# Kernel tuning notes

Hardware: AMD Instinct MI355X
Metric: run time of the kernel (lower is better)

The kernel has to match this reference:

```python
import jax, jax.numpy as jnp
import numpy as np

B, P, K = 32, 1024, 20  # clouds, points per cloud, kNN neighbors
EPS = 1e-5


def knn_idx(x, k):
    # x: [B,P,d] -> indices of k nearest neighbors (squared L2, includes self), [B,P,k]
    d2 = jnp.sum(x * x, axis=-1)
    dist = d2[:, :, None] + d2[:, None, :] - 2.0 * jnp.einsum('bpd,bqd->bpq', x, x)
    _, idx = jax.lax.top_k(-dist, k)
    return idx


def edge_conv(x, idx, msg_fn):
    # gather neighbor features, build [x_i, x_j - x_i] edge features, max-aggregate
    xj = jax.vmap(lambda xb, ib: xb[ib])(x, idx)            # [B,P,K,d]
    xi = jnp.broadcast_to(x[:, :, None, :], xj.shape)       # [B,P,K,d]
    e = jnp.concatenate([xi, xj - xi], axis=-1)             # [B,P,K,2d]
    return jnp.max(msg_fn(e), axis=2)                       # [B,P,out]


def setup_inputs() -> dict:
    key = jax.random.key(0)
    ks = jax.random.split(key, 5)
    s = 0.05
    return {
        'pos': jax.random.normal(ks[0], (B * P, 3), jnp.float32),
        'W1a': jax.random.normal(ks[1], (6, 64), jnp.float32) * s,
        'b1a': jnp.zeros((64,), jnp.float32),
        'g1': jnp.ones((64,), jnp.float32),
        'be1': jnp.zeros((64,), jnp.float32),
        'W1b': jax.random.normal(ks[2], (64, 64), jnp.float32) * s,
        'b1b': jnp.zeros((64,), jnp.float32),
        'W2': jax.random.normal(ks[3], (128, 128), jnp.float32) * s,
        'b2': jnp.zeros((128,), jnp.float32),
        'Wl': jax.random.normal(ks[4], (192, 128), jnp.float32) * s,
        'bl': jnp.zeros((128,), jnp.float32),
        'batch': jnp.repeat(jnp.arange(B, dtype=jnp.int32), P),
    }


def reference(pos, W1a, b1a, g1, be1, W1b, b1b, W2, b2, Wl, bl, batch):
    # batch is uniform-sized and sorted -> fixed reshape to [B,P,.]
    x0 = pos.reshape(B, P, 3)

    def mlp1(e):  # Linear(6,64) -> BatchNorm -> ReLU -> Linear(64,64)
        h = e @ W1a + b1a
        mu = jnp.mean(h, axis=(0, 1, 2))
        var = jnp.var(h, axis=(0, 1, 2))
        h = (h - mu) * jax.lax.rsqrt(var + EPS) * g1 + be1
        h = jax.nn.relu(h)
        return h @ W1b + b1b

    x1 = edge_conv(x0, knn_idx(x0, K), mlp1)                         # [B,P,64]
    x2 = edge_conv(x1, knn_idx(x1, K), lambda e: e @ W2 + b2)        # [B,P,128]
    h = jnp.concatenate([x1, x2], axis=-1) @ Wl + bl                 # [B,P,128]
    return jnp.max(h, axis=1)                                        # global_max_pool -> [B,128]
```

## Files before the change

kernel.cpp:

```cpp
#include <hip/hip_runtime.h>
#include <cfloat>
#include <cstdint>

#define NB 32
#define NP 1024
#define NK 20
#define NPTS 32768

typedef __attribute__((ext_vector_type(8))) short bf16x8;
typedef __attribute__((ext_vector_type(4))) float f32x4;

__device__ __forceinline__ unsigned bf16rne(float v) {
  const unsigned u = __float_as_uint(v);
  return (u + 0x7fffu + ((u >> 16) & 1u)) >> 16;
}

__device__ __forceinline__ float unsort_f(unsigned s) {
  const unsigned m = (~(unsigned)((int)s >> 31)) | 0x80000000u;
  return __uint_as_float(s ^ m);
}

__global__ __launch_bounds__(256) void kd2(const float* __restrict__ x, int dim,
                                           float* __restrict__ d2) {
  int p = blockIdx.x * 256 + threadIdx.x;
  if (p >= NPTS) return;
  if (dim == 64) {
    const float4* xr = (const float4*)(x + (size_t)p * 64);
    float s = 0.f;
#pragma unroll
    for (int dq = 0; dq < 16; dq++) {
      float4 v = xr[dq];
      s = fmaf(v.x, v.x, s);
      s = fmaf(v.y, v.y, s);
      s = fmaf(v.z, v.z, s);
      s = fmaf(v.w, v.w, s);
    }
    d2[p] = s;
  } else {
    float s = 0.f;
#pragma unroll
    for (int d = 0; d < 3; d++) {
      float v = x[p * 3 + d];
      s = fmaf(v, v, s);
    }
    d2[p] = s;
  }
}

__global__ __launch_bounds__(256) void kxprep(const float* __restrict__ x,
                                              unsigned short* __restrict__ Xh,
                                              unsigned short* __restrict__ Xl) {
  const int t = blockIdx.x * 256 + threadIdx.x;
  const int p = t >> 3, g = t & 7;
  const float4* xr = (const float4*)(x + (size_t)p * 64 + g * 8);
  const float4 v0 = xr[0];
  const float4 v1 = xr[1];
  const float vv[8] = {v0.x, v0.y, v0.z, v0.w, v1.x, v1.y, v1.z, v1.w};
  unsigned short h[8], l[8];
#pragma unroll
  for (int j = 0; j < 8; j++) {
    const float z = vv[j];
    const unsigned u = __float_as_uint(z);
    const unsigned hb = (u + 0x7fffu + ((u >> 16) & 1u)) & 0xffff0000u;
    h[j] = (unsigned short)(hb >> 16);
    l[j] = (unsigned short)bf16rne(z - __uint_as_float(hb));
  }
  const int off = (((p >> 4) * 2 + (g >> 2)) * 64 + ((g & 3) << 4) + (p & 15)) * 8;
  *(uint4*)&Xh[off] = *(const uint4*)&h[0];
  *(uint4*)&Xl[off] = *(const uint4*)&l[0];
}

__global__ __launch_bounds__(256) void kdistm(const unsigned short* __restrict__ Xh,
                                              const unsigned short* __restrict__ Xl,
                                              const float* __restrict__ d2,
                                              int c0, int nc, float* __restrict__ D) {
  const int lane = threadIdx.x & 63;
  const int w = threadIdx.x >> 6;
  const int cloud = blockIdx.x % nc;
  const int t = blockIdx.x / nc;
  const int tr0 = (t >> 3) * 128, tc0 = (t & 7) * 128;
  const int cb = (c0 + cloud) * 1024;
  const int rw = tr0 + w * 32;

  bf16x8 Ah[2][2], Al[2][2];
#pragma unroll
  for (int mt = 0; mt < 2; mt++)
#pragma unroll
    for (int ks = 0; ks < 2; ks++) {
      const int tg = (cb + rw + mt * 16) >> 4;
      const size_t base = ((size_t)(tg * 2 + ks) * 64 + lane) * 8;
      Ah[mt][ks] = *(const bf16x8*)&Xh[base];
      Al[mt][ks] = *(const bf16x8*)&Xl[base];
    }
  float d2r[2][4];
#pragma unroll
  for (int mt = 0; mt < 2; mt++)
#pragma unroll
    for (int r = 0; r < 4; r++)
      d2r[mt][r] = d2[cb + rw + mt * 16 + (lane >> 4) * 4 + r];

  for (int nt = 0; nt < 8; nt++) {
    const int cg = cb + tc0 + nt * 16;
    bf16x8 Bh2[2], Bl2[2];
#pragma unroll
    for (int ks = 0; ks < 2; ks++) {
      const int tg = cg >> 4;
      const size_t base = ((size_t)(tg * 2 + ks) * 64 + lane) * 8;
      Bh2[ks] = *(const bf16x8*)&Xh[base];
      Bl2[ks] = *(const bf16x8*)&Xl[base];
    }
    const float d2c = d2[cg + (lane & 15)];
#pragma unroll
    for (int mt = 0; mt < 2; mt++) {
      f32x4 C = {0.f, 0.f, 0.f, 0.f};
      C = __builtin_amdgcn_mfma_f32_16x16x32_bf16(Ah[mt][0], Bh2[0], C, 0, 0, 0);
      C = __builtin_amdgcn_mfma_f32_16x16x32_bf16(Ah[mt][0], Bl2[0], C, 0, 0, 0);
      C = __builtin_amdgcn_mfma_f32_16x16x32_bf16(Al[mt][0], Bh2[0], C, 0, 0, 0);
      C = __builtin_amdgcn_mfma_f32_16x16x32_bf16(Ah[mt][1], Bh2[1], C, 0, 0, 0);
      C = __builtin_amdgcn_mfma_f32_16x16x32_bf16(Ah[mt][1], Bl2[1], C, 0, 0, 0);
      C = __builtin_amdgcn_mfma_f32_16x16x32_bf16(Al[mt][1], Bh2[1], C, 0, 0, 0);
#pragma unroll
      for (int r = 0; r < 4; r++) {
        const int row = cloud * 1024 + rw + mt * 16 + (lane >> 4) * 4 + r;
        const int col = tc0 + nt * 16 + (lane & 15);
        D[(size_t)row * 1024 + col] = fmaf(-2.f, C[r], d2r[mt][r] + d2c);
      }
    }
  }
}

__device__ __forceinline__ void select20(const float* dv, unsigned long long* w,
                                         int lane, int pg, int gbase,
                                         int* __restrict__ idxo) {
  unsigned k32[16];
#pragma unroll
  for (int ii = 0; ii < 16; ii++) {
    unsigned u = __float_as_uint(dv[ii]);
    u ^= (((int)u >> 31) | 0x80000000u);
    k32[ii] = u;
  }
  unsigned lmn = k32[0];
#pragma unroll
  for (int ii = 1; ii < 16; ii++) lmn = k32[ii] < lmn ? k32[ii] : lmn;
  unsigned mn = lmn, mlm = lmn;
#pragma unroll
  for (int s = 1; s < 64; s <<= 1) {
    const unsigned a = __shfl_xor(mn, s, 64);
    const unsigned b = __shfl_xor(mlm, s, 64);
    mn = a < mn ? a : mn;
    mlm = b > mlm ? b : mlm;
  }
  unsigned lo32 = mn;
  unsigned long long hi32 = (unsigned long long)mlm + 1;
  float flo = unsort_f(mn), fhi = unsort_f(mlm);
  float clo = 0.f, chi = 140.f;
  unsigned m32 = 0;
  bool found = false;
  for (int it = 0; it < 40; ++it) {
    if (hi32 - (unsigned long long)lo32 <= 1) break;
    unsigned m;
    if (it < 6) {
      float fr = (42.f - clo) / (chi - clo);
      fr = fr < 0.04f ? 0.04f : (fr > 0.96f ? 0.96f : fr);
      const float pf = fmaf(fhi - flo, fr, flo);
      unsigned u = __float_as_uint(pf);
      u ^= (((int)u >> 31) | 0x80000000u);
      m = u;
      if (m <= lo32) m = lo32 + 1;
      if ((unsigned long long)m >= hi32) m = (unsigned)(hi32 - 1);
    } else {
      m = (unsigned)(lo32 + ((hi32 - lo32) >> 1));
    }
    int cnt = 0;
#pragma unroll
    for (int ii = 0; ii < 16; ii++) cnt += __popcll(__ballot(k32[ii] < m));
    if (cnt < 20) {
      lo32 = m;
      flo = unsort_f(m);
      clo = (float)cnt;
    } else if (cnt > 64) {
      hi32 = m;
      fhi = unsort_f(m);
      chi = (float)cnt;
    } else {
      m32 = m;
      found = true;
      break;
    }
  }

  if (found) {
    unsigned mask = 0;
#pragma unroll
    for (int ii = 0; ii < 16; ii++) mask |= (k32[ii] < m32) ? (1u << ii) : 0u;
    const int lc = __popc(mask);
    int x = lc;
#pragma unroll
    for (int s = 1; s < 64; s <<= 1) {
      const int y = __shfl_up(x, s, 64);
      if (lane >= s) x += y;
    }
    int off = x - lc;
    w[lane] = ~0ULL;
    __builtin_amdgcn_wave_barrier();
#pragma unroll
    for (int i = 0; i < 4; i++)
#pragma unroll
      for (int j = 0; j < 4; j++) {
        const int ii = i * 4 + j;
        if ((mask & (1u << ii)) && off < 64) {
          w[off] = ((unsigned long long)k32[ii] << 10) |
                   (unsigned)(i * 256 + (lane << 2) + j);
          off++;
        }
      }
    __builtin_amdgcn_wave_barrier();
    unsigned long long K = w[lane];
#pragma unroll
    for (int k = 2; k <= 64; k <<= 1) {
#pragma unroll
      for (int j2 = k >> 1; j2 > 0; j2 >>= 1) {
        const unsigned long long o = __shfl_xor(K, j2, 64);
        const bool takeMin = (((lane & j2) == 0) == ((lane & k) == 0));
        const bool lt = K < o;
        const unsigned long long sml = lt ? K : o;
        const unsigned long long big = lt ? o : K;
        K = takeMin ? sml : big;
      }
    }
    if (lane < NK) idxo[(size_t)pg * NK + lane] = gbase + (int)(K & 1023u);
  } else {
    unsigned long long lo64 = ((unsigned long long)lo32) << 10;
    unsigned long long hi64 = hi32 << 10;
    unsigned long long cut = hi64;
    for (int it = 0; it < 48 && (hi64 - lo64) > 1; ++it) {
      const unsigned long long m = lo64 + ((hi64 - lo64) >> 1);
      int cnt = 0;
#pragma unroll
      for (int ii = 0; ii < 16; ii++) {
        const unsigned long long key =
            ((unsigned long long)k32[ii] << 10) |
            (unsigned)(((ii >> 2) << 8) + (lane << 2) + (ii & 3));
        cnt += __popcll(__ballot(key < m));
      }
      if (cnt == 20) {
        cut = m;
        break;
      }
      if (cnt < 20)
        lo64 = m;
      else
        hi64 = m;
      cut = hi64;
    }
    int base = 0;
#pragma unroll
    for (int ii = 0; ii < 16; ii++) {
      const unsigned long long key =
          ((unsigned long long)k32[ii] << 10) |
          (unsigned)(((ii >> 2) << 8) + (lane << 2) + (ii & 3));
      const unsigned long long b = __ballot(key < cut);
      if (key < cut) {
        const int slot = base + __builtin_amdgcn_mbcnt_hi(
                                    (unsigned)(b >> 32),
                                    __builtin_amdgcn_mbcnt_lo((unsigned)b, 0));
        idxo[(size_t)pg * NK + slot] = gbase + (int)(key & 1023u);
      }
      base += __popcll(b);
    }
  }
}

__global__ __launch_bounds__(512) void kfsel1(const float* __restrict__ pos,
                                              const float* __restrict__ d2,
                                              int* __restrict__ idxo) {
  __shared__ float px[1024], py[1024], pz[1024], pd2[1024];
  __shared__ unsigned long long lw[8][64];
  const int tid = threadIdx.x;
  const int lane = tid & 63;
  const int w = tid >> 6;
  const int cloud = blockIdx.x >> 7;
  const int mb = blockIdx.x & 127;
  const int cb = cloud << 10;

  if (tid < 256) {
    const float4* ppos = (const float4*)(pos + (size_t)cb * 3 + tid * 12);
    const float4 a = ppos[0], b = ppos[1], c = ppos[2];
    *(float4*)&px[tid * 4] = make_float4(a.x, a.w, b.z, c.y);
    *(float4*)&py[tid * 4] = make_float4(a.y, b.x, b.w, c.z);
    *(float4*)&pz[tid * 4] = make_float4(a.z, b.y, c.x, c.w);
  }
  *(float2*)&pd2[tid * 2] = *(const float2*)(d2 + cb + tid * 2);
  __syncthreads();

  const int pl = mb * 8 + w;
  const float xi0 = px[pl], xi1 = py[pl], xi2 = pz[pl];
  const float dp = pd2[pl];
  float dv[16];
#pragma unroll
  for (int i = 0; i < 4; i++) {
    const float4 X = *(const float4*)&px[i * 256 + lane * 4];
    const float4 Y = *(const float4*)&py[i * 256 + lane * 4];
    const float4 Z = *(const float4*)&pz[i * 256 + lane * 4];
    const float4 Q = *(const float4*)&pd2[i * 256 + lane * 4];
    const float xs[4] = {X.x, X.y, X.z, X.w};
    const float ys[4] = {Y.x, Y.y, Y.z, Y.w};
    const float zs[4] = {Z.x, Z.y, Z.z, Z.w};
    const float qs[4] = {Q.x, Q.y, Q.z, Q.w};
#pragma unroll
    for (int j = 0; j < 4; j++) {
      float acc = 0.f;
      acc = fmaf(xi0, xs[j], acc);
      acc = fmaf(xi1, ys[j], acc);
      acc = fmaf(xi2, zs[j], acc);
      dv[i * 4 + j] = fmaf(-2.f, acc, dp + qs[j]);
    }
  }
  select20(dv, lw[w], lane, cb + pl, cb, idxo);
}

__global__ __launch_bounds__(256) void kselect2(const float* __restrict__ D,
                                                int c0, int* __restrict__ idxo) {
  __shared__ unsigned long long lw[4][64];
  const int lane = threadIdx.x & 63;
  const int sub = threadIdx.x >> 6;
  const int pchunk = blockIdx.x * 4 + sub;
  const int pg = c0 * 1024 + pchunk;
  const int gbase = (pg >> 10) << 10;

  float dv[16];
  const float4* dr = (const float4*)(D + (size_t)pchunk * 1024 + lane * 4);
#pragma unroll
  for (int i = 0; i < 4; i++) {
    const float4 d4 = dr[i * 64];
    dv[i * 4 + 0] = d4.x;
    dv[i * 4 + 1] = d4.y;
    dv[i * 4 + 2] = d4.z;
    dv[i * 4 + 3] = d4.w;
  }
  select20(dv, lw[sub], lane, pg, gbase, idxo);
}

__global__ __launch_bounds__(256) void kstats(const float* __restrict__ pos,
                                              const int* __restrict__ idx,
                                              double* __restrict__ Spart) {
  __shared__ float red[4][42];
  const int tid = threadIdx.x;
  const int w = tid >> 6;
  int p = blockIdx.x * 256 + tid;
  float xi0 = pos[p * 3], xi1 = pos[p * 3 + 1], xi2 = pos[p * 3 + 2];
  float s1[6];
  float s2[36];
#pragma unroll
  for (int a = 0; a < 6; a++) s1[a] = 0.f;
#pragma unroll
  for (int a = 0; a < 36; a++) s2[a] = 0.f;
  for (int k = 0; k < NK; k++) {
    int j = idx[p * NK + k];
    float e[6];
    e[0] = xi0;
    e[1] = xi1;
    e[2] = xi2;
    e[3] = pos[j * 3] - xi0;
    e[4] = pos[j * 3 + 1] - xi1;
    e[5] = pos[j * 3 + 2] - xi2;
#pragma unroll
    for (int a = 0; a < 6; a++) {
      s1[a] += e[a];
#pragma unroll
      for (int b = 0; b < 6; b++) s2[a * 6 + b] = fmaf(e[a], e[b], s2[a * 6 + b]);
    }
  }
#pragma unroll
  for (int a = 0; a < 6; a++) {
#pragma unroll
    for (int m = 1; m < 64; m <<= 1) s1[a] += __shfl_xor(s1[a], m, 64);
  }
#pragma unroll
  for (int a = 0; a < 36; a++) {
#pragma unroll
    for (int m = 1; m < 64; m <<= 1) s2[a] += __shfl_xor(s2[a], m, 64);
  }
  if ((tid & 63) == 0) {
#pragma unroll
    for (int a = 0; a < 6; a++) red[w][a] = s1[a];
#pragma unroll
    for (int a = 0; a < 36; a++) red[w][6 + a] = s2[a];
  }
  __syncthreads();
  if (tid < 42) {
    double t = (double)red[0][tid] + (double)red[1][tid] + (double)red[2][tid] +
               (double)red[3][tid];
    Spart[(size_t)blockIdx.x * 42 + tid] = t;
  }
}

__global__ void kbn(const double* __restrict__ Spart, const float* __restrict__ W1a,
                    const float* __restrict__ b1a, const float* __restrict__ g1,
                    const float* __restrict__ be1, const float* __restrict__ W1b,
                    float* __restrict__ ss, unsigned short* __restrict__ Bh,
                    unsigned short* __restrict__ Bl) {
  __shared__ double S[42];
  const int c = threadIdx.x;
  if (c < 42) {
    double t = 0.0;
    for (int b = 0; b < 128; b++) t += Spart[(size_t)b * 42 + c];
    S[c] = t;
  }
  for (int t = c; t < 4096; t += 256) {
    const int j = t & 7, L = (t >> 3) & 63, f = t >> 9;
    const int nt = f >> 1, ks = f & 1;
    const int k = ks * 32 + (L >> 4) * 8 + j;
    const int n = nt * 16 + (L & 15);
    const float wv = W1b[k * 64 + n];
    const unsigned u = __float_as_uint(wv);
    const unsigned hb = (u + 0x7fffu + ((u >> 16) & 1u)) & 0xffff0000u;
    Bh[t] = (unsigned short)(hb >> 16);
    Bl[t] = (unsigned short)bf16rne(wv - __uint_as_float(hb));
  }
  __syncthreads();
  if (c < 64) {
    double w[6];
#pragma unroll
    for (int d = 0; d < 6; d++) w[d] = (double)W1a[d * 64 + c];
    double b = (double)b1a[c];
    const double invN = 1.0 / (double)((size_t)NPTS * NK);
    double m1 = 0.0;
#pragma unroll
    for (int d = 0; d < 6; d++) m1 += w[d] * S[d];
    m1 *= invN;
    double q = 0.0;
#pragma unroll
    for (int a = 0; a < 6; a++)
#pragma unroll
      for (int d = 0; d < 6; d++) q += w[a] * w[d] * S[6 + a * 6 + d];
    q *= invN;
    double mu = m1 + b;
    double eh2 = q + 2.0 * b * m1 + b * b;
    double var = eh2 - mu * mu;
    if (var < 0.0) var = 0.0;
    double inv = 1.0 / sqrt(var + 1e-5);
    double sc = (double)g1[c] * inv;
    ss[c] = (float)sc;
    ss[64 + c] = (float)((double)be1[c] - mu * sc);
  }
}

#define EC1P 8
__global__ __launch_bounds__(256) void kec1(const float* __restrict__ pos,
                                            const int* __restrict__ idx,
                                            const float* __restrict__ ss,
                                            const float* __restrict__ W1a,
                                            const float* __restrict__ b1a,
                                            const unsigned short* __restrict__ Bh,
                                            const unsigned short* __restrict__ Bl,
                                            const float* __restrict__ b1b,
                                            float* __restrict__ x1) {
  __shared__ __align__(16) unsigned short Ah[4][3072];
  __shared__ __align__(16) unsigned short Al[4][3072];
  __shared__ float nbr[4][160];
  const int tid = threadIdx.x;
  const int lane = tid & 63;
  const int w = tid >> 6;
  const int p0 = blockIdx.x * EC1P + w * 2;

  unsigned short* ah = Ah[w];
  unsigned short* al = Al[w];
  float* nb = nbr[w];

  if (lane < 40) {
    const int j = idx[(size_t)p0 * NK + lane];
    nb[lane * 4 + 0] = pos[j * 3 + 0];
    nb[lane * 4 + 1] = pos[j * 3 + 1];
    nb[lane * 4 + 2] = pos[j * 3 + 2];
  }

  float wdf[3], wbt[3];
#pragma unroll
  for (int d = 0; d < 3; d++) {
    const float top = W1a[d * 64 + lane];
    const float bot = W1a[(3 + d) * 64 + lane];
    wdf[d] = top - bot;
    wbt[d] = bot;
  }
  const float b1 = b1a[lane];
  const float sc = ss[lane];
  const float sh = ss[64 + lane];
  const int lanepart = ((lane >> 5) * 512) + (((lane & 31) >> 3) * 128) + (lane & 7);
  __builtin_amdgcn_wave_barrier();

#pragma unroll
  for (int pp = 0; pp < 2; pp++) {
    const int p = p0 + pp;
    const float xi0 = pos[p * 3], xi1 = pos[p * 3 + 1], xi2 = pos[p * 3 + 2];
    const float pu = fmaf(xi2, wdf[2], fmaf(xi1, wdf[1], fmaf(xi0, wdf[0], b1)));
    for (int k = 0; k < NK; k++) {
      const int row = pp * NK + k;
      const float4 nbv = *(const float4*)&nb[row * 4];
      const float pv = fmaf(nbv.z, wbt[2], fmaf(nbv.y, wbt[1], nbv.x * wbt[0]));
      const float z = fmaxf(fmaf(pu + pv, sc, sh), 0.f);
      const unsigned u = __float_as_uint(z);
      const unsigned hb = (u + 0x7fffu + ((u >> 16) & 1u)) & 0xffff0000u;
      const int off = (row >> 4) * 1024 + (row & 15) * 8 + lanepart;
      ah[off] = (unsigned short)(hb >> 16);
      al[off] = (unsigned short)bf16rne(z - __uint_as_float(hb));
    }
  }
  __builtin_amdgcn_wave_barrier();

  bf16x8 bh[4][2], bl[4][2];
#pragma unroll
  for (int nt = 0; nt < 4; nt++)
#pragma unroll
    for (int ks = 0; ks < 2; ks++) {
      const int base = ((nt * 2 + ks) * 64 + lane) * 8;
      bh[nt][ks] = *(const bf16x8*)&Bh[base];
      bl[nt][ks] = *(const bf16x8*)&Bl[base];
    }

  float pA[4], pB[4];
#pragma unroll
  for (int nt = 0; nt < 4; nt++) {
    pA[nt] = -FLT_MAX;
    pB[nt] = -FLT_MAX;
  }
  const int q4 = (lane >> 4) * 4;

#pragma unroll
  for (int mt = 0; mt < 3; mt++) {
    const bf16x8 a_h0 = *(const bf16x8*)&ah[mt * 1024 + lane * 8];
    const bf16x8 a_l0 = *(const bf16x8*)&al[mt * 1024 + lane * 8];
    const bf16x8 a_h1 = *(const bf16x8*)&ah[mt * 1024 + 512 + lane * 8];
    const bf16x8 a_l1 = *(const bf16x8*)&al[mt * 1024 + 512 + lane * 8];
#pragma unroll
    for (int nt = 0; nt < 4; nt++) {
      f32x4 C = {0.f, 0.f, 0.f, 0.f};
      C = __builtin_amdgcn_mfma_f32_16x16x32_bf16(a_h0, bh[nt][0], C, 0, 0, 0);
      C = __builtin_amdgcn_mfma_f32_16x16x32_bf16(a_h0, bl[nt][0], C, 0, 0, 0);
      C = __builtin_amdgcn_mfma_f32_16x16x32_bf16(a_l0, bh[nt][0], C, 0, 0, 0);
      C = __builtin_amdgcn_mfma_f32_16x16x32_bf16(a_h1, bh[nt][1], C, 0, 0, 0);
      C = __builtin_amdgcn_mfma_f32_16x16x32_bf16(a_h1, bl[nt][1], C, 0, 0, 0);
      C = __builtin_amdgcn_mfma_f32_16x16x32_bf16(a_l1, bh[nt][1], C, 0, 0, 0);
#pragma unroll
      for (int r = 0; r < 4; r++) {
        const int row = mt * 16 + q4 + r;
        const float vv = C[r];
        if (row < NK) pA[nt] = fmaxf(pA[nt], vv);
        if (row >= NK && row < 2 * NK) pB[nt] = fmaxf(pB[nt], vv);
      }
    }
  }
#pragma unroll
  for (int s = 16; s < 64; s <<= 1) {
#pragma unroll
    for (int nt = 0; nt < 4; nt++) {
      pA[nt] = fmaxf(pA[nt], __shfl_xor(pA[nt], s, 64));
      pB[nt] = fmaxf(pB[nt], __shfl_xor(pB[nt], s, 64));
    }
  }
  if (lane < 16) {
#pragma unroll
    for (int nt = 0; nt < 4; nt++) {
      const float bb = b1b[nt * 16 + lane];
      x1[(size_t)p0 * 64 + nt * 16 + lane] = pA[nt] + bb;
      x1[(size_t)(p0 + 1) * 64 + nt * 16 + lane] = pB[nt] + bb;
    }
  }
}

__global__ __launch_bounds__(256) void kv(const float* __restrict__ x1,
                                          const float* __restrict__ W2,
                                          float* __restrict__ v) {
  const int c = threadIdx.x & 127;
  const int sub = threadIdx.x >> 7;
  float wv[64];
#pragma unroll
  for (int d = 0; d < 64; d++) wv[d] = W2[(64 + d) * 128 + c];
  const int pbase = blockIdx.x * 64 + sub * 32;
  for (int i = 0; i < 32; i++) {
    const int p = pbase + i;
    const float4* xr = (const float4*)(x1 + (size_t)p * 64);
    float a0 = 0.f, a1 = 0.f;
#pragma unroll
    for (int dq = 0; dq < 16; dq++) {
      float4 xv = xr[dq];
      a0 = fmaf(xv.x, wv[dq * 4 + 0], a0);
      a1 = fmaf(xv.y, wv[dq * 4 + 1], a1);
      a0 = fmaf(xv.z, wv[dq * 4 + 2], a0);
      a1 = fmaf(xv.w, wv[dq * 4 + 3], a1);
    }
    v[(size_t)p * 128 + c] = a0 + a1;
  }
}

__global__ __launch_bounds__(256) void kprep(const float* __restrict__ W2,
                                             const float* __restrict__ Wl,
                                             const float* __restrict__ b2,
                                             const float* __restrict__ bl,
                                             float* __restrict__ Bc,
                                             float* __restrict__ cb) {
  const int t = blockIdx.x * 256 + threadIdx.x;
  const int d = t >> 7, c = t & 127;
  float s = Wl[d * 128 + c];
  for (int e = 0; e < 128; e++)
    s = fmaf(W2[d * 128 + e] - W2[(64 + d) * 128 + e], Wl[(64 + e) * 128 + c], s);
  Bc[d * 128 + c] = s;
  Bc[(64 + 2 * d) * 128 + c] = Wl[(64 + 2 * d) * 128 + c];
  Bc[(64 + 2 * d + 1) * 128 + c] = Wl[(64 + 2 * d + 1) * 128 + c];
  if (d == 0) {
    float sb = bl[c];
    for (int e = 0; e < 128; e++) sb = fmaf(b2[e], Wl[(64 + e) * 128 + c], sb);
    cb[c] = sb;
  }
}

__global__ __launch_bounds__(256) void kprep2(const float* __restrict__ Bc,
                                              unsigned short* __restrict__ Bch,
                                              unsigned short* __restrict__ Bcl) {
  const int t = blockIdx.x * 256 + threadIdx.x;
  const int j = t & 7, L = (t >> 3) & 63, f = t >> 9;
  const int nt = f / 6, kc = f % 6;
  const int k = kc * 32 + ((L >> 4) << 3) + j;
  const int n = nt * 16 + (L & 15);
  const float wv = Bc[k * 128 + n];
  const unsigned u = __float_as_uint(wv);
  const unsigned hb = (u + 0x7fffu + ((u >> 16) & 1u)) & 0xffff0000u;
  Bch[t] = (unsigned short)(hb >> 16);
  Bcl[t] = (unsigned short)bf16rne(wv - __uint_as_float(hb));
}

__global__ __launch_bounds__(256) void kgemm(const float* __restrict__ x1,
                                             const float* __restrict__ v,
                                             const int* __restrict__ idx,
                                             const unsigned short* __restrict__ Bch,
                                             const unsigned short* __restrict__ Bcl,
                                             float* __restrict__ partial) {
  __shared__ __align__(16) unsigned short Ah[12288];
  __shared__ __align__(16) unsigned short Al[12288];
  __shared__ int idxs[1280];
  __shared__ float red[4][8][16];
  const int tid = threadIdx.x;
  const int lane = tid & 63;
  const int w = tid >> 6;
  const int cloud = blockIdx.x & 31;
  const int mb = blockIdx.x >> 5;
  const int pbase = cloud * 1024 + mb * 64;
  const int mrow = lane & 15, gsel = lane >> 4;

#pragma unroll
  for (int r = 0; r < 5; r++) {
    const int id = r * 256 + tid;
    idxs[id] = idx[(size_t)pbase * NK + id];
  }

#pragma unroll
  for (int rr = 0; rr < 2; rr++) {
    const int mt = w, kc = rr;
    const int m = mt * 16 + mrow;
    const float4* xr =
        (const float4*)(x1 + (size_t)(pbase + m) * 64 + kc * 32 + gsel * 8);
    const float4 v0 = xr[0], v1 = xr[1];
    const float vv[8] = {v0.x, v0.y, v0.z, v0.w, v1.x, v1.y, v1.z, v1.w};
    unsigned short h8[8], l8[8];
#pragma unroll
    for (int j = 0; j < 8; j++) {
      const unsigned u = __float_as_uint(vv[j]);
      const unsigned hb = (u + 0x7fffu + ((u >> 16) & 1u)) & 0xffff0000u;
      h8[j] = (unsigned short)(hb >> 16);
      l8[j] = (unsigned short)bf16rne(vv[j] - __uint_as_float(hb));
    }
    const int a16 = (mt * 6 + kc) * 64 + lane;
    *(uint4*)&Ah[a16 * 8] = *(const uint4*)h8;
    *(uint4*)&Al[a16 * 8] = *(const uint4*)l8;
  }
  __syncthreads();

#pragma unroll
  for (int rr = 0; rr < 4; rr++) {
    const int i3 = rr * 4 + w;
    const int mt = i3 & 3, kg_hi = i3 >> 2;
    const int m = mt * 16 + mrow;
    const int kk0 = (kg_hi * 4 + gsel) * 8;
    const int* ip = &idxs[m * NK];
    float mx[8];
#pragma unroll
    for (int j = 0; j < 8; j++) mx[j] = -FLT_MAX;
    for (int k = 0; k < NK; k++) {
      const float4* vr = (const float4*)(v + (size_t)ip[k] * 128 + kk0);
      const float4 a = vr[0], b = vr[1];
      mx[0] = fmaxf(mx[0], a.x);
      mx[1] = fmaxf(mx[1], a.y);
      mx[2] = fmaxf(mx[2], a.z);
      mx[3] = fmaxf(mx[3], a.w);
      mx[4] = fmaxf(mx[4], b.x);
      mx[5] = fmaxf(mx[5], b.y);
      mx[6] = fmaxf(mx[6], b.z);
      mx[7] = fmaxf(mx[7], b.w);
    }
    unsigned short h8[8], l8[8];
#pragma unroll
    for (int j = 0; j < 8; j++) {
      const unsigned u = __float_as_uint(mx[j]);
      const unsigned hb = (u + 0x7fffu + ((u >> 16) & 1u)) & 0xffff0000u;
      h8[j] = (unsigned short)(hb >> 16);
      l8[j] = (unsigned short)bf16rne(mx[j] - __uint_as_float(hb));
    }
    const int a16 = (mt * 6 + 2 + kg_hi) * 64 + lane;
    *(uint4*)&Ah[a16 * 8] = *(const uint4*)h8;
    *(uint4*)&Al[a16 * 8] = *(const uint4*)l8;
  }
  __syncthreads();

  f32x4 acc[8];
#pragma unroll
  for (int nt = 0; nt < 8; nt++) acc[nt] = {0.f, 0.f, 0.f, 0.f};
  const int mt = w;
#pragma unroll
  for (int kc = 0; kc < 6; kc++) {
    const int a16 = (mt * 6 + kc) * 64 + lane;
    const bf16x8 a_h = *(const bf16x8*)&Ah[a16 * 8];
    const bf16x8 a_l = *(const bf16x8*)&Al[a16 * 8];
#pragma unroll
    for (int nt = 0; nt < 8; nt++) {
      const size_t bo = ((size_t)(nt * 6 + kc) * 64 + lane) * 8;
      const bf16x8 b_h = *(const bf16x8*)&Bch[bo];
      const bf16x8 b_l = *(const bf16x8*)&Bcl[bo];
      acc[nt] = __builtin_amdgcn_mfma_f32_16x16x32_bf16(a_h, b_h, acc[nt], 0, 0, 0);
      acc[nt] = __builtin_amdgcn_mfma_f32_16x16x32_bf16(a_h, b_l, acc[nt], 0, 0, 0);
      acc[nt] = __builtin_amdgcn_mfma_f32_16x16x32_bf16(a_l, b_h, acc[nt], 0, 0, 0);
      acc[nt] = __builtin_amdgcn_mfma_f32_16x16x32_bf16(a_l, b_l, acc[nt], 0, 0, 0);
    }
  }

#pragma unroll
  for (int nt = 0; nt < 8; nt++) {
    float rm = fmaxf(fmaxf(acc[nt][0], acc[nt][1]), fmaxf(acc[nt][2], acc[nt][3]));
    rm = fmaxf(rm, __shfl_xor(rm, 16, 64));
    rm = fmaxf(rm, __shfl_xor(rm, 32, 64));
    if (lane < 16) red[w][nt][lane] = rm;
  }
  __syncthreads();
  if (tid < 128) {
    const int nt = tid >> 4, cc = tid & 15;
    const float m4 = fmaxf(fmaxf(red[0][nt][cc], red[1][nt][cc]),
                           fmaxf(red[2][nt][cc], red[3][nt][cc]));
    partial[(size_t)(cloud * 16 + mb) * 128 + tid] = m4;
  }
}

__global__ __launch_bounds__(256) void kred(const float* __restrict__ partial,
                                            const float* __restrict__ cb,
                                            float* __restrict__ out) {
  int t = blockIdx.x * 256 + threadIdx.x;
  int b = t >> 7, c = t & 127;
  float m = -FLT_MAX;
#pragma unroll
  for (int mb = 0; mb < 16; mb++) m = fmaxf(m, partial[(size_t)(b * 16 + mb) * 128 + c]);
  out[t] = m + cb[c];
}

extern "C" void kernel_launch(void* const* d_in, const int* in_sizes, int n_in,
                              void* d_out, int out_size, void* d_ws, size_t ws_size,
                              hipStream_t stream) {
  const float* pos = (const float*)d_in[0];
  const float* W1a = (const float*)d_in[1];
  const float* b1a = (const float*)d_in[2];
  const float* g1 = (const float*)d_in[3];
  const float* be1 = (const float*)d_in[4];
  const float* W1b = (const float*)d_in[5];
  const float* b1b = (const float*)d_in[6];
  const float* W2 = (const float*)d_in[7];
  const float* b2 = (const float*)d_in[8];
  const float* Wl = (const float*)d_in[9];
  const float* bl = (const float*)d_in[10];
  float* out = (float*)d_out;

  float* ws = (float*)d_ws;
  float* x1 = ws;
  float* v = ws + 2097152;
  int* idx = (int*)(ws + 6291456);
  float* d2b = ws + 6946816;
  double* Spart = (double*)(ws + 6979584);
  float* Bc = ws + 6990336;
  float* cb = ws + 7014912;
  float* ss = ws + 7015040;
  unsigned short* Bh = (unsigned short*)(ws + 7015168);
  unsigned short* Bl = (unsigned short*)(ws + 7017216);
  float* partial = ws + 7019264;
  unsigned short* Xfh = (unsigned short*)(ws + 7084800);
  unsigned short* Xfl = (unsigned short*)(ws + 8133376);
  unsigned short* Bch2 = (unsigned short*)(ws + 9181952);
  unsigned short* Bcl2 = (unsigned short*)(ws + 9194240);
  const size_t base = 9206528;
  float* D = ws + base;

  if (ws_size < (base + 1024 * 1024) * sizeof(float)) return;

  size_t avail = ws_size / sizeof(float) - base;
  int nc = 1;
  for (int c = 32; c >= 1; c >>= 1)
    if ((size_t)c * 1024 * 1024 <= avail) {
      nc = c;
      break;
    }

  kd2<<<128, 256, 0, stream>>>(pos, 3, d2b);
  kfsel1<<<NB * 128, 512, 0, stream>>>(pos, d2b, idx);

  kstats<<<128, 256, 0, stream>>>(pos, idx, Spart);
  kbn<<<1, 256, 0, stream>>>(Spart, W1a, b1a, g1, be1, W1b, ss, Bh, Bl);
  kec1<<<NPTS / EC1P, 256, 0, stream>>>(pos, idx, ss, W1a, b1a, Bh, Bl, b1b, x1);

  kd2<<<128, 256, 0, stream>>>(x1, 64, d2b);
  kxprep<<<1024, 256, 0, stream>>>(x1, Xfh, Xfl);
  for (int c0 = 0; c0 < NB; c0 += nc) {
    kdistm<<<nc * 64, 256, 0, stream>>>(Xfh, Xfl, d2b, c0, nc, D);
    kselect2<<<nc * 256, 256, 0, stream>>>(D, c0, idx);
  }

  kv<<<512, 256, 0, stream>>>(x1, W2, v);
  kprep<<<32, 256, 0, stream>>>(W2, Wl, b2, bl, Bc, cb);
  kprep2<<<96, 256, 0, stream>>>(Bc, Bch2, Bcl2);
  kgemm<<<512, 256, 0, stream>>>(x1, v, idx, Bch2, Bcl2, partial);
  kred<<<16, 256, 0, stream>>>(partial, cb, out);
}
```

Measured before the change: 354.2 us.

## Keep gemm A fragments in registers and drop low-low bf16 product

```diff
diff --git a/kernel.cpp b/kernel.cpp
--- a/kernel.cpp
+++ b/kernel.cpp
@@ -635,9 +635,7 @@
                                              const unsigned short* __restrict__ Bch,
                                              const unsigned short* __restrict__ Bcl,
                                              float* __restrict__ partial) {
-  __shared__ __align__(16) unsigned short Ah[12288];
-  __shared__ __align__(16) unsigned short Al[12288];
-  __shared__ int idxs[1280];
+  __shared__ int idxs[4][320];
   __shared__ float red[4][8][16];
   const int tid = threadIdx.x;
   const int lane = tid & 63;
@@ -646,89 +644,82 @@
   const int mb = blockIdx.x >> 5;
   const int pbase = cloud * 1024 + mb * 64;
   const int mrow = lane & 15, gsel = lane >> 4;
-
-#pragma unroll
-  for (int r = 0; r < 5; r++) {
-    const int id = r * 256 + tid;
-    idxs[id] = idx[(size_t)pbase * NK + id];
-  }
-
-#pragma unroll
-  for (int rr = 0; rr < 2; rr++) {
-    const int mt = w, kc = rr;
-    const int m = mt * 16 + mrow;
+  const int m = w * 16 + mrow;
+
+#pragma unroll
+  for (int r = 0; r < 5; r++)
+    idxs[w][r * 64 + lane] = idx[(size_t)(pbase + w * 16) * NK + r * 64 + lane];
+  __builtin_amdgcn_wave_barrier();
+
+  bf16x8 aH[6], aL[6];
+#pragma unroll
+  for (int kc = 0; kc < 2; kc++) {
     const float4* xr =
         (const float4*)(x1 + (size_t)(pbase + m) * 64 + kc * 32 + gsel * 8);
     const float4 v0 = xr[0], v1 = xr[1];
     const float vv[8] = {v0.x, v0.y, v0.z, v0.w, v1.x, v1.y, v1.z, v1.w};
-    unsigned short h8[8], l8[8];
+    bf16x8 h, l;
 #pragma unroll
     for (int j = 0; j < 8; j++) {
       const unsigned u = __float_as_uint(vv[j]);
       const unsigned hb = (u + 0x7fffu + ((u >> 16) & 1u)) & 0xffff0000u;
-      h8[j] = (unsigned short)(hb >> 16);
-      l8[j] = (unsigned short)bf16rne(vv[j] - __uint_as_float(hb));
-    }
-    const int a16 = (mt * 6 + kc) * 64 + lane;
-    *(uint4*)&Ah[a16 * 8] = *(const uint4*)h8;
-    *(uint4*)&Al[a16 * 8] = *(const uint4*)l8;
-  }
-  __syncthreads();
-
-#pragma unroll
-  for (int rr = 0; rr < 4; rr++) {
-    const int i3 = rr * 4 + w;
-    const int mt = i3 & 3, kg_hi = i3 >> 2;
-    const int m = mt * 16 + mrow;
-    const int kk0 = (kg_hi * 4 + gsel) * 8;
-    const int* ip = &idxs[m * NK];
-    float mx[8];
-#pragma unroll
-    for (int j = 0; j < 8; j++) mx[j] = -FLT_MAX;
-    for (int k = 0; k < NK; k++) {
-      const float4* vr = (const float4*)(v + (size_t)ip[k] * 128 + kk0);
-      const float4 a = vr[0], b = vr[1];
-      mx[0] = fmaxf(mx[0], a.x);
-      mx[1] = fmaxf(mx[1], a.y);
-      mx[2] = fmaxf(mx[2], a.z);
-      mx[3] = fmaxf(mx[3], a.w);
-      mx[4] = fmaxf(mx[4], b.x);
-      mx[5] = fmaxf(mx[5], b.y);
-      mx[6] = fmaxf(mx[6], b.z);
-      mx[7] = fmaxf(mx[7], b.w);
-    }
-    unsigned short h8[8], l8[8];
+      h[j] = (short)(hb >> 16);
+      l[j] = (short)bf16rne(vv[j] - __uint_as_float(hb));
+    }
+    aH[kc] = h;
+    aL[kc] = l;
+  }
+
+  float mx[4][8];
+#pragma unroll
+  for (int g = 0; g < 4; g++)
+#pragma unroll
+    for (int j = 0; j < 8; j++) mx[g][j] = -FLT_MAX;
+  const int* ips = &idxs[w][mrow * NK];
+#pragma unroll 5
+  for (int k = 0; k < NK; k++) {
+    const float* vr = v + (size_t)ips[k] * 128 + gsel * 8;
+#pragma unroll
+    for (int g = 0; g < 4; g++) {
+      const float4 a = *(const float4*)(vr + g * 32);
+      const float4 b = *(const float4*)(vr + g * 32 + 4);
+      mx[g][0] = fmaxf(mx[g][0], a.x);
+      mx[g][1] = fmaxf(mx[g][1], a.y);
+      mx[g][2] = fmaxf(mx[g][2], a.z);
+      mx[g][3] = fmaxf(mx[g][3], a.w);
+      mx[g][4] = fmaxf(mx[g][4], b.x);
+      mx[g][5] = fmaxf(mx[g][5], b.y);
+      mx[g][6] = fmaxf(mx[g][6], b.z);
+      mx[g][7] = fmaxf(mx[g][7], b.w);
+    }
+  }
+#pragma unroll
+  for (int g = 0; g < 4; g++) {
+    bf16x8 h, l;
 #pragma unroll
     for (int j = 0; j < 8; j++) {
-      const unsigned u = __float_as_uint(mx[j]);
+      const unsigned u = __float_as_uint(mx[g][j]);
       const unsigned hb = (u + 0x7fffu + ((u >> 16) & 1u)) & 0xffff0000u;
-      h8[j] = (unsigned short)(hb >> 16);
-      l8[j] = (unsigned short)bf16rne(mx[j] - __uint_as_float(hb));
-    }
-    const int a16 = (mt * 6 + 2 + kg_hi) * 64 + lane;
-    *(uint4*)&Ah[a16 * 8] = *(const uint4*)h8;
-    *(uint4*)&Al[a16 * 8] = *(const uint4*)l8;
-  }
-  __syncthreads();
+      h[j] = (short)(hb >> 16);
+      l[j] = (short)bf16rne(mx[g][j] - __uint_as_float(hb));
+    }
+    aH[2 + g] = h;
+    aL[2 + g] = l;
+  }
 
   f32x4 acc[8];
 #pragma unroll
   for (int nt = 0; nt < 8; nt++) acc[nt] = {0.f, 0.f, 0.f, 0.f};
-  const int mt = w;
-#pragma unroll
-  for (int kc = 0; kc < 6; kc++) {
-    const int a16 = (mt * 6 + kc) * 64 + lane;
-    const bf16x8 a_h = *(const bf16x8*)&Ah[a16 * 8];
-    const bf16x8 a_l = *(const bf16x8*)&Al[a16 * 8];
-#pragma unroll
-    for (int nt = 0; nt < 8; nt++) {
+#pragma unroll
+  for (int nt = 0; nt < 8; nt++) {
+#pragma unroll
+    for (int kc = 0; kc < 6; kc++) {
       const size_t bo = ((size_t)(nt * 6 + kc) * 64 + lane) * 8;
       const bf16x8 b_h = *(const bf16x8*)&Bch[bo];
       const bf16x8 b_l = *(const bf16x8*)&Bcl[bo];
-      acc[nt] = __builtin_amdgcn_mfma_f32_16x16x32_bf16(a_h, b_h, acc[nt], 0, 0, 0);
-      acc[nt] = __builtin_amdgcn_mfma_f32_16x16x32_bf16(a_h, b_l, acc[nt], 0, 0, 0);
-      acc[nt] = __builtin_amdgcn_mfma_f32_16x16x32_bf16(a_l, b_h, acc[nt], 0, 0, 0);
-      acc[nt] = __builtin_amdgcn_mfma_f32_16x16x32_bf16(a_l, b_l, acc[nt], 0, 0, 0);
+      acc[nt] = __builtin_amdgcn_mfma_f32_16x16x32_bf16(aH[kc], b_h, acc[nt], 0, 0, 0);
+      acc[nt] = __builtin_amdgcn_mfma_f32_16x16x32_bf16(aH[kc], b_l, acc[nt], 0, 0, 0);
+      acc[nt] = __builtin_amdgcn_mfma_f32_16x16x32_bf16(aL[kc], b_h, acc[nt], 0, 0, 0);
     }
   }
 
```

New measurement: 346.4 us. 2.2% less time.
